# Kernel optimization log

Measured on AMD Instinct MI355X. Metric: run time of the kernel, lower is better.

The kernel has to match this reference:

```python
import jax, jax.numpy as jnp
import numpy as np


def setup_inputs() -> dict:
    key = jax.random.key(0)
    ks = jax.random.split(key, 6)
    b, t, k, h = 2, 2048, 256, 8
    s = 1.0 / np.sqrt(k)
    return {
        "x": jax.random.normal(ks[0], (b, t, k), dtype=jnp.float32),
        "Wq": jax.random.normal(ks[1], (k, k * h), dtype=jnp.float32) * s,
        "Wk": jax.random.normal(ks[2], (k, k * h), dtype=jnp.float32) * s,
        "Wv": jax.random.normal(ks[3], (k, k * h), dtype=jnp.float32) * s,
        "Wu": jax.random.normal(ks[4], (k * h, k), dtype=jnp.float32) * (1.0 / np.sqrt(k * h)),
        "bu": jnp.zeros((k,), dtype=jnp.float32),
    }


def reference(x, Wq, Wk, Wv, Wu, bu):
    b, t, k = x.shape
    h = Wq.shape[1] // k
    scale = k ** (-0.25)
    # projections -> [b, t, h, k] -> [b, h, t, k]
    q = (x @ Wq).reshape(b, t, h, k).transpose(0, 2, 1, 3) * scale
    kk = (x @ Wk).reshape(b, t, h, k).transpose(0, 2, 1, 3) * scale
    v = (x @ Wv).reshape(b, t, h, k).transpose(0, 2, 1, 3)
    dot = jnp.einsum('bhqk,bhsk->bhqs', q, kk)  # [b,h,t,t]
    attn = jax.nn.softmax(dot, axis=-1)
    out = jnp.einsum('bhqs,bhsk->bhqk', attn, v)  # [b,h,t,k]
    out = out.transpose(0, 2, 1, 3).reshape(b, t, h * k)
    return out @ Wu + bu
```

## Files before the change

### kernel.cpp

```cpp
#include <hip/hip_runtime.h>

using bf16x8   = __bf16 __attribute__((ext_vector_type(8)));
using floatx4  = float __attribute__((ext_vector_type(4)));
using floatx16 = float __attribute__((ext_vector_type(16)));

static __device__ __forceinline__ unsigned short f2b(float x) {
  unsigned u = __builtin_bit_cast(unsigned, x);
  u = (u + 0x7fffu + ((u >> 16) & 1u)) >> 16;
  return (unsigned short)u;
}

static __device__ __forceinline__ void gl_lds16(const unsigned short* g, unsigned short* l) {
  __builtin_amdgcn_global_load_lds((const __attribute__((address_space(1))) void*)g,
                                   (__attribute__((address_space(3))) void*)l, 16, 0, 0);
}

__global__ __launch_bounds__(256) void prep_kernel(const float* __restrict__ x,
                                                   const float* __restrict__ Wq,
                                                   const float* __restrict__ Wk,
                                                   const float* __restrict__ Wv,
                                                   const float* __restrict__ Wu,
                                                   unsigned short* __restrict__ xb,
                                                   unsigned short* __restrict__ wqkt,
                                                   unsigned short* __restrict__ wvt,
                                                   unsigned short* __restrict__ wut) {
  int bx = blockIdx.x;
  if (bx < 1024) {
    int i = (bx * 256 + threadIdx.x) * 4;
    float4 v = *(const float4*)(x + i);
    unsigned long long p = (unsigned long long)f2b(v.x) |
                           ((unsigned long long)f2b(v.y) << 16) |
                           ((unsigned long long)f2b(v.z) << 32) |
                           ((unsigned long long)f2b(v.w) << 48);
    *(unsigned long long*)(xb + i) = p;
    return;
  }
  __shared__ unsigned short T[64][65];
  const float* src;
  unsigned short* dst;
  int R, C, tile;
  if (bx < 1152)      { src = Wq; dst = wqkt;          R = 256;  C = 2048; tile = bx - 1024; }
  else if (bx < 1280) { src = Wk; dst = wqkt + 524288; R = 256;  C = 2048; tile = bx - 1152; }
  else if (bx < 1408) { src = Wv; dst = wvt;           R = 256;  C = 2048; tile = bx - 1280; }
  else                { src = Wu; dst = wut;           R = 2048; C = 256;  tile = bx - 1408; }
  int ctiles = C >> 6;
  int cx = tile % ctiles, ry = tile / ctiles;
  int r0 = ry * 64, c0 = cx * 64;
  int t = threadIdx.x;
#pragma unroll
  for (int i = 0; i < 16; ++i) {
    int idx = i * 256 + t;
    int r = idx >> 6, c = idx & 63;
    T[r][c] = f2b(src[(size_t)(r0 + r) * C + c0 + c]);
  }
  __syncthreads();
#pragma unroll
  for (int i = 0; i < 16; ++i) {
    int idx = i * 256 + t;
    int c = idx >> 6, r = idx & 63;
    dst[(size_t)(c0 + c) * R + r0 + r] = T[r][c];
  }
}

__global__ __launch_bounds__(256) void proj_kernel(const unsigned short* __restrict__ A,
                                                   const unsigned short* __restrict__ Bt,
                                                   unsigned short* __restrict__ qkb,
                                                   unsigned short* __restrict__ vtb) {
  __shared__ __align__(16) unsigned short SMEM[128 * 136];
  unsigned short* As = SMEM;
  unsigned short* Bs = SMEM + 4096;
  const int Kt = 256;
  int tid = threadIdx.x, lane = tid & 63, w = tid >> 6;
  int m16 = lane & 15, quad = lane >> 4;
  int wr = w & 1, wc = w >> 1;
  int m0 = blockIdx.y * 128, n0 = blockIdx.x * 128;
  int srow0 = w * 32 + (lane >> 2);
  int schunk = (lane & 3) ^ ((lane >> 2) & 3);
  floatx4 acc[4][4] = {};
  for (int k0 = 0; k0 < Kt; k0 += 32) {
    __syncthreads();
#pragma unroll
    for (int j = 0; j < 2; ++j) {
      int r = srow0 + j * 16;
      gl_lds16(A + (size_t)(m0 + r) * Kt + k0 + schunk * 8, &As[(w * 32 + j * 16) * 32]);
      gl_lds16(Bt + (size_t)(n0 + r) * Kt + k0 + schunk * 8, &Bs[(w * 32 + j * 16) * 32]);
    }
    __syncthreads();
    int sw = (quad ^ (m16 & 3)) * 8;
    bf16x8 af[4], bfr[4];
#pragma unroll
    for (int i = 0; i < 4; ++i) {
      af[i]  = *(const bf16x8*)(&As[(wr * 64 + i * 16 + m16) * 32 + sw]);
      bfr[i] = *(const bf16x8*)(&Bs[(wc * 64 + i * 16 + m16) * 32 + sw]);
    }
#pragma unroll
    for (int i = 0; i < 4; ++i)
#pragma unroll
      for (int jn = 0; jn < 4; ++jn)
        acc[i][jn] = __builtin_amdgcn_mfma_f32_16x16x32_bf16(af[i], bfr[jn], acc[i][jn], 0, 0, 0);
  }
  if (n0 < 4096) {
#pragma unroll
    for (int i = 0; i < 4; ++i)
#pragma unroll
      for (int jn = 0; jn < 4; ++jn)
#pragma unroll
        for (int r = 0; r < 4; ++r) {
          int m = m0 + wr * 64 + i * 16 + quad * 4 + r;
          int n = n0 + wc * 64 + jn * 16 + m16;
          qkb[(size_t)m * 4096 + n] = f2b(acc[i][jn][r]);
        }
  } else {
    __syncthreads();
    unsigned short* Vt = SMEM;
#pragma unroll
    for (int i = 0; i < 4; ++i)
#pragma unroll
      for (int jn = 0; jn < 4; ++jn)
#pragma unroll
        for (int r = 0; r < 4; ++r) {
          int nn = wc * 64 + jn * 16 + m16;
          int mm = wr * 64 + i * 16 + quad * 4 + r;
          Vt[nn * 136 + mm] = f2b(acc[i][jn][r]);
        }
    __syncthreads();
    int bb = m0 >> 11, t0 = m0 & 2047;
#pragma unroll
    for (int i2 = 0; i2 < 8; ++i2) {
      int idx = i2 * 256 + tid;
      int nn = idx >> 4;
      int mc = (idx & 15) * 8;
      uint4 v = *(const uint4*)(&Vt[nn * 136 + mc]);
      *(uint4*)(&vtb[((size_t)(bb * 2048 + n0 - 4096 + nn)) * 2048 + t0 + mc]) = v;
    }
  }
}

__global__ __launch_bounds__(256) void out_kernel(const unsigned short* __restrict__ A,
                                                  const unsigned short* __restrict__ Bt,
                                                  float* __restrict__ Cout,
                                                  const float* __restrict__ bias) {
  __shared__ unsigned short As[64 * 64];
  __shared__ unsigned short Bs[64 * 64];
  const int Kt = 2048;
  int tid = threadIdx.x, lane = tid & 63, w = tid >> 6;
  int m16 = lane & 15, quad = lane >> 4;
  int m0 = blockIdx.y * 64, n0 = blockIdx.x * 64;
  int srow_i = lane >> 3;
  int schunk = (lane & 7) ^ srow_i;
  int rsw = m16 & 7;
  floatx4 acc[4] = {};
  for (int k0 = 0; k0 < Kt; k0 += 64) {
    __syncthreads();
#pragma unroll
    for (int j = 0; j < 2; ++j) {
      int r = w * 16 + j * 8 + srow_i;
      gl_lds16(A + (size_t)(m0 + r) * Kt + k0 + schunk * 8, &As[(w * 16 + j * 8) * 64]);
      gl_lds16(Bt + (size_t)(n0 + r) * Kt + k0 + schunk * 8, &Bs[(w * 16 + j * 8) * 64]);
    }
    __syncthreads();
    bf16x8 af[2];
#pragma unroll
    for (int kk = 0; kk < 2; ++kk)
      af[kk] = *(const bf16x8*)(&As[(w * 16 + m16) * 64 + (((kk * 4 + quad) ^ rsw) * 8)]);
#pragma unroll
    for (int nt = 0; nt < 4; ++nt)
#pragma unroll
      for (int kk = 0; kk < 2; ++kk) {
        bf16x8 bfv = *(const bf16x8*)(&Bs[(nt * 16 + m16) * 64 + (((kk * 4 + quad) ^ rsw) * 8)]);
        acc[nt] = __builtin_amdgcn_mfma_f32_16x16x32_bf16(af[kk], bfv, acc[nt], 0, 0, 0);
      }
  }
#pragma unroll
  for (int nt = 0; nt < 4; ++nt)
#pragma unroll
    for (int r = 0; r < 4; ++r) {
      int m = m0 + w * 16 + quad * 4 + r;
      int n = n0 + nt * 16 + m16;
      Cout[(size_t)m * 256 + n] = acc[nt][r] + bias[n];
    }
}

__global__ __launch_bounds__(512, 2) void attn_kernel(const unsigned short* __restrict__ qk,
                                                      const unsigned short* __restrict__ vt,
                                                      unsigned short* __restrict__ ao) {
  __shared__ __align__(16) unsigned short Ks[2][64 * 256];
  __shared__ __align__(16) unsigned short Vs[2][256 * 64];
  __shared__ __align__(16) unsigned short Pb[4][32 * 72];
  int tid = threadIdx.x, lane = tid & 63, w = tid >> 6;
  int c32 = lane & 31, hi = lane >> 5;
  int qg = w & 3, u = w >> 2;
  int id = blockIdx.x;
  int xcd = id & 7, j = id >> 3;
  int bh = xcd + 8 * (j & 1);
  int q0 = (j >> 1) * 128;
  int b = bh >> 3, h = bh & 7;

  bf16x8 qf[16];
  const unsigned short* qrow =
      qk + (size_t)(b * 2048 + q0 + qg * 32 + c32) * 4096 + h * 256 + hi * 8;
#pragma unroll
  for (int kk = 0; kk < 16; ++kk) qf[kk] = *(const bf16x8*)(qrow + kk * 16);

  bf16x8 onesf;
#pragma unroll
  for (int i = 0; i < 8; ++i) onesf[i] = (__bf16)1.0f;

  floatx16 O[4] = {};
  floatx16 l = {};

  const unsigned short* kbase = qk + (size_t)b * 2048 * 4096 + 2048 + h * 256;
  const unsigned short* vbase = vt + (size_t)bh * 256 * 2048;
  unsigned short* pq = &Pb[qg][0];

  int krow_i = lane >> 5, kpos = lane & 31;
  int vrow_i = lane >> 3, vpos = lane & 7;
  int ksw = c32 & 7;

#pragma unroll
  for (int i = 0; i < 4; ++i) {
    int kr = i * 2 + krow_i;
    gl_lds16(kbase + (size_t)(w * 8 + kr) * 4096 + ((kpos ^ (kr & 7)) * 8),
             &Ks[0][(w * 8 + i * 2) * 256]);
    int vr = i * 8 + vrow_i;
    gl_lds16(vbase + (size_t)(w * 32 + vr) * 2048 + ((vpos ^ vrow_i) * 8),
             &Vs[0][(w * 32 + i * 8) * 64]);
  }

  for (int st = 0; st < 32; ++st) {
    int cur = st & 1;
    __syncthreads();

    floatx16 s = {};
    const unsigned short* krl = &Ks[cur][(u * 32 + c32) * 256];
#pragma unroll
    for (int kk = 0; kk < 16; ++kk) {
      bf16x8 kf = *(const bf16x8*)(krl + (((kk * 2 + hi) ^ ksw) * 8));
      s = __builtin_amdgcn_mfma_f32_32x32x16_bf16(qf[kk], kf, s, 0, 0, 0);
    }
#pragma unroll
    for (int i = 0; i < 16; ++i) {
      float p = __expf(s[i] * 0.0625f);
      int q = (i & 3) + 8 * (i >> 2) + 4 * hi;
      pq[q * 72 + u * 32 + c32] = f2b(p);
    }
    __syncthreads();

    if (st < 31) {
      int s0 = (st + 1) * 64;
      unsigned short* kdst = &Ks[1 - cur][0];
      unsigned short* vdst = &Vs[1 - cur][0];
#pragma unroll
      for (int i = 0; i < 4; ++i) {
        int kr = i * 2 + krow_i;
        gl_lds16(kbase + (size_t)(s0 + w * 8 + kr) * 4096 + ((kpos ^ (kr & 7)) * 8),
                 kdst + (w * 8 + i * 2) * 256);
        int vr = i * 8 + vrow_i;
        gl_lds16(vbase + (size_t)(w * 32 + vr) * 2048 + s0 + ((vpos ^ vrow_i) * 8),
                 vdst + (w * 32 + i * 8) * 64);
      }
    }

    bf16x8 paf[4];
#pragma unroll
    for (int f = 0; f < 4; ++f) paf[f] = *(const bf16x8*)(pq + c32 * 72 + f * 16 + hi * 8);
#pragma unroll
    for (int f = 0; f < 4; ++f)
      l = __builtin_amdgcn_mfma_f32_32x32x16_bf16(paf[f], onesf, l, 0, 0, 0);
#pragma unroll
    for (int dt = 0; dt < 4; ++dt) {
      const unsigned short* vrl = &Vs[cur][(u * 128 + dt * 32 + c32) * 64];
#pragma unroll
      for (int f = 0; f < 4; ++f) {
        bf16x8 vf = *(const bf16x8*)(vrl + (((f * 2 + hi) ^ ksw) * 8));
        O[dt] = __builtin_amdgcn_mfma_f32_32x32x16_bf16(paf[f], vf, O[dt], 0, 0, 0);
      }
    }
  }
  float inv[16];
#pragma unroll
  for (int i = 0; i < 16; ++i) inv[i] = 1.0f / l[i];
#pragma unroll
  for (int dt = 0; dt < 4; ++dt)
#pragma unroll
    for (int i = 0; i < 16; ++i) {
      int q = (i & 3) + 8 * (i >> 2) + 4 * hi;
      ao[(size_t)(b * 2048 + q0 + qg * 32 + q) * 2048 + h * 256 + u * 128 + dt * 32 + c32] =
          f2b(O[dt][i] * inv[i]);
    }
}

extern "C" void kernel_launch(void* const* d_in, const int* in_sizes, int n_in,
                              void* d_out, int out_size, void* d_ws, size_t ws_size,
                              hipStream_t stream) {
  const float* x  = (const float*)d_in[0];
  const float* Wq = (const float*)d_in[1];
  const float* Wk = (const float*)d_in[2];
  const float* Wv = (const float*)d_in[3];
  const float* Wu = (const float*)d_in[4];
  const float* bu = (const float*)d_in[5];

  unsigned short* xb   = (unsigned short*)d_ws;
  unsigned short* wqkt = xb + 1048576;
  unsigned short* wvt  = wqkt + 1048576;
  unsigned short* wut  = wvt + 524288;
  unsigned short* qkb  = wut + 524288;
  unsigned short* vtb  = qkb + 16777216;
  unsigned short* aob  = vtb + 8388608;

  prep_kernel<<<1536, 256, 0, stream>>>(x, Wq, Wk, Wv, Wu, xb, wqkt, wvt, wut);
  proj_kernel<<<dim3(48, 32), 256, 0, stream>>>(xb, wqkt, qkb, vtb);
  attn_kernel<<<256, 512, 0, stream>>>(qkb, vtb, aob);
  out_kernel<<<dim3(4, 64), 256, 0, stream>>>(aob, wut, (float*)d_out, bu);
}
```

Before: 200.9 us.

## Split attention keys across warp pairs and deepen out-GEMM K tile

Measured after the change: 201.3 us. No clear change (+0.2%).

```diff
diff --git a/kernel.cpp b/kernel.cpp
--- a/kernel.cpp
+++ b/kernel.cpp
@@ -140,34 +140,34 @@
                                                   const unsigned short* __restrict__ Bt,
                                                   float* __restrict__ Cout,
                                                   const float* __restrict__ bias) {
-  __shared__ unsigned short As[64 * 64];
-  __shared__ unsigned short Bs[64 * 64];
+  __shared__ unsigned short As[64 * 128];
+  __shared__ unsigned short Bs[64 * 128];
   const int Kt = 2048;
   int tid = threadIdx.x, lane = tid & 63, w = tid >> 6;
   int m16 = lane & 15, quad = lane >> 4;
   int m0 = blockIdx.y * 64, n0 = blockIdx.x * 64;
-  int srow_i = lane >> 3;
-  int schunk = (lane & 7) ^ srow_i;
+  int srow_i = lane >> 4;
+  int spos = lane & 15;
   int rsw = m16 & 7;
   floatx4 acc[4] = {};
-  for (int k0 = 0; k0 < Kt; k0 += 64) {
-    __syncthreads();
-#pragma unroll
-    for (int j = 0; j < 2; ++j) {
-      int r = w * 16 + j * 8 + srow_i;
-      gl_lds16(A + (size_t)(m0 + r) * Kt + k0 + schunk * 8, &As[(w * 16 + j * 8) * 64]);
-      gl_lds16(Bt + (size_t)(n0 + r) * Kt + k0 + schunk * 8, &Bs[(w * 16 + j * 8) * 64]);
-    }
-    __syncthreads();
-    bf16x8 af[2];
-#pragma unroll
-    for (int kk = 0; kk < 2; ++kk)
-      af[kk] = *(const bf16x8*)(&As[(w * 16 + m16) * 64 + (((kk * 4 + quad) ^ rsw) * 8)]);
+  for (int k0 = 0; k0 < Kt; k0 += 128) {
+    __syncthreads();
+#pragma unroll
+    for (int j = 0; j < 4; ++j) {
+      int r = w * 16 + j * 4 + srow_i;
+      gl_lds16(A + (size_t)(m0 + r) * Kt + k0 + ((spos ^ (r & 7)) * 8), &As[(w * 16 + j * 4) * 128]);
+      gl_lds16(Bt + (size_t)(n0 + r) * Kt + k0 + ((spos ^ (r & 7)) * 8), &Bs[(w * 16 + j * 4) * 128]);
+    }
+    __syncthreads();
+    bf16x8 af[4];
+#pragma unroll
+    for (int kk = 0; kk < 4; ++kk)
+      af[kk] = *(const bf16x8*)(&As[(w * 16 + m16) * 128 + (((kk * 4 + quad) ^ rsw) * 8)]);
 #pragma unroll
     for (int nt = 0; nt < 4; ++nt)
 #pragma unroll
-      for (int kk = 0; kk < 2; ++kk) {
-        bf16x8 bfv = *(const bf16x8*)(&Bs[(nt * 16 + m16) * 64 + (((kk * 4 + quad) ^ rsw) * 8)]);
+      for (int kk = 0; kk < 4; ++kk) {
+        bf16x8 bfv = *(const bf16x8*)(&Bs[(nt * 16 + m16) * 128 + (((kk * 4 + quad) ^ rsw) * 8)]);
         acc[nt] = __builtin_amdgcn_mfma_f32_16x16x32_bf16(af[kk], bfv, acc[nt], 0, 0, 0);
       }
   }
@@ -184,12 +184,14 @@
 __global__ __launch_bounds__(512, 2) void attn_kernel(const unsigned short* __restrict__ qk,
                                                       const unsigned short* __restrict__ vt,
                                                       unsigned short* __restrict__ ao) {
-  __shared__ __align__(16) unsigned short Ks[2][64 * 256];
-  __shared__ __align__(16) unsigned short Vs[2][256 * 64];
-  __shared__ __align__(16) unsigned short Pb[4][32 * 72];
+  __shared__ __align__(16) unsigned char SM[150016];
+  unsigned short* KsBuf = (unsigned short*)SM;
+  unsigned short* VsBuf = (unsigned short*)(SM + 65536);
+  float* lsh = (float*)(SM + 149504);
   int tid = threadIdx.x, lane = tid & 63, w = tid >> 6;
   int c32 = lane & 31, hi = lane >> 5;
   int qg = w & 3, u = w >> 2;
+  unsigned short* Pw = (unsigned short*)(SM + 131072) + w * 1152;
   int id = blockIdx.x;
   int xcd = id & 7, j = id >> 3;
   int bh = xcd + 8 * (j & 1);
@@ -202,16 +204,11 @@
 #pragma unroll
   for (int kk = 0; kk < 16; ++kk) qf[kk] = *(const bf16x8*)(qrow + kk * 16);
 
-  bf16x8 onesf;
-#pragma unroll
-  for (int i = 0; i < 8; ++i) onesf[i] = (__bf16)1.0f;
-
-  floatx16 O[4] = {};
-  floatx16 l = {};
+  floatx16 O[8] = {};
+  float lacc = 0.f;
 
   const unsigned short* kbase = qk + (size_t)b * 2048 * 4096 + 2048 + h * 256;
   const unsigned short* vbase = vt + (size_t)bh * 256 * 2048;
-  unsigned short* pq = &Pb[qg][0];
 
   int krow_i = lane >> 5, kpos = lane & 31;
   int vrow_i = lane >> 3, vpos = lane & 7;
@@ -221,73 +218,93 @@
   for (int i = 0; i < 4; ++i) {
     int kr = i * 2 + krow_i;
     gl_lds16(kbase + (size_t)(w * 8 + kr) * 4096 + ((kpos ^ (kr & 7)) * 8),
-             &Ks[0][(w * 8 + i * 2) * 256]);
+             KsBuf + (w * 8 + i * 2) * 256);
     int vr = i * 8 + vrow_i;
     gl_lds16(vbase + (size_t)(w * 32 + vr) * 2048 + ((vpos ^ vrow_i) * 8),
-             &Vs[0][(w * 32 + i * 8) * 64]);
+             VsBuf + (w * 32 + i * 8) * 64);
   }
 
   for (int st = 0; st < 32; ++st) {
     int cur = st & 1;
-    __syncthreads();
-
-    floatx16 s = {};
-    const unsigned short* krl = &Ks[cur][(u * 32 + c32) * 256];
-#pragma unroll
-    for (int kk = 0; kk < 16; ++kk) {
-      bf16x8 kf = *(const bf16x8*)(krl + (((kk * 2 + hi) ^ ksw) * 8));
-      s = __builtin_amdgcn_mfma_f32_32x32x16_bf16(qf[kk], kf, s, 0, 0, 0);
-    }
-#pragma unroll
-    for (int i = 0; i < 16; ++i) {
-      float p = __expf(s[i] * 0.0625f);
-      int q = (i & 3) + 8 * (i >> 2) + 4 * hi;
-      pq[q * 72 + u * 32 + c32] = f2b(p);
-    }
-    __syncthreads();
-
+    unsigned short* Kc = KsBuf + cur * 16384;
+    unsigned short* Vc = VsBuf + cur * 16384;
+    __syncthreads();
     if (st < 31) {
       int s0 = (st + 1) * 64;
-      unsigned short* kdst = &Ks[1 - cur][0];
-      unsigned short* vdst = &Vs[1 - cur][0];
+      unsigned short* kd = KsBuf + (1 - cur) * 16384;
+      unsigned short* vd = VsBuf + (1 - cur) * 16384;
 #pragma unroll
       for (int i = 0; i < 4; ++i) {
         int kr = i * 2 + krow_i;
         gl_lds16(kbase + (size_t)(s0 + w * 8 + kr) * 4096 + ((kpos ^ (kr & 7)) * 8),
-                 kdst + (w * 8 + i * 2) * 256);
+                 kd + (w * 8 + i * 2) * 256);
         int vr = i * 8 + vrow_i;
         gl_lds16(vbase + (size_t)(w * 32 + vr) * 2048 + s0 + ((vpos ^ vrow_i) * 8),
-                 vdst + (w * 32 + i * 8) * 64);
-      }
-    }
-
-    bf16x8 paf[4];
-#pragma unroll
-    for (int f = 0; f < 4; ++f) paf[f] = *(const bf16x8*)(pq + c32 * 72 + f * 16 + hi * 8);
-#pragma unroll
-    for (int f = 0; f < 4; ++f)
-      l = __builtin_amdgcn_mfma_f32_32x32x16_bf16(paf[f], onesf, l, 0, 0, 0);
-#pragma unroll
-    for (int dt = 0; dt < 4; ++dt) {
-      const unsigned short* vrl = &Vs[cur][(u * 128 + dt * 32 + c32) * 64];
-#pragma unroll
-      for (int f = 0; f < 4; ++f) {
-        bf16x8 vf = *(const bf16x8*)(vrl + (((f * 2 + hi) ^ ksw) * 8));
+                 vd + (w * 32 + i * 8) * 64);
+      }
+    }
+
+    floatx16 s = {};
+    const unsigned short* krl = Kc + (u * 32 + c32) * 256;
+#pragma unroll
+    for (int kk = 0; kk < 16; ++kk) {
+      bf16x8 kf = *(const bf16x8*)(krl + (((kk * 2 + hi) ^ ksw) * 8));
+      s = __builtin_amdgcn_mfma_f32_32x32x16_bf16(kf, qf[kk], s, 0, 0, 0);
+    }
+    float lsum = 0.f;
+#pragma unroll
+    for (int i = 0; i < 16; ++i) {
+      float p = __expf(s[i] * 0.0625f);
+      lsum += p;
+      int sl = (i & 3) + 8 * (i >> 2) + 4 * hi;
+      Pw[c32 * 36 + sl] = f2b(p);
+    }
+    lacc += lsum;
+    bf16x8 paf[2];
+#pragma unroll
+    for (int f = 0; f < 2; ++f) paf[f] = *(const bf16x8*)(Pw + c32 * 36 + f * 16 + hi * 8);
+#pragma unroll
+    for (int dt = 0; dt < 8; ++dt) {
+      const unsigned short* vrl = Vc + (dt * 32 + c32) * 64;
+#pragma unroll
+      for (int f = 0; f < 2; ++f) {
+        bf16x8 vf = *(const bf16x8*)(vrl + (((u * 4 + f * 2 + hi) ^ ksw) * 8));
         O[dt] = __builtin_amdgcn_mfma_f32_32x32x16_bf16(paf[f], vf, O[dt], 0, 0, 0);
       }
     }
   }
-  float inv[16];
-#pragma unroll
-  for (int i = 0; i < 16; ++i) inv[i] = 1.0f / l[i];
-#pragma unroll
-  for (int dt = 0; dt < 4; ++dt)
+
+  float lw = lacc + __shfl_xor(lacc, 32);
+  __syncthreads();
+  float* osh = (float*)SM;
+  if (u == 0) {
+    float* od = osh + qg * 8192;
+#pragma unroll
+    for (int dt = 0; dt < 8; ++dt)
+#pragma unroll
+      for (int i = 0; i < 16; ++i) {
+        int q = (i & 3) + 8 * (i >> 2) + 4 * hi;
+        od[q * 256 + dt * 32 + c32] = O[dt][i];
+      }
+    if (hi == 0) lsh[qg * 32 + c32] = lw;
+  }
+  __syncthreads();
+  if (u == 1 && hi == 0) lsh[qg * 32 + c32] += lw;
+  __syncthreads();
+  if (u == 1) {
+    float* od = osh + qg * 8192;
+    unsigned short* aor = ao + (size_t)(b * 2048 + q0 + qg * 32) * 2048 + h * 256;
 #pragma unroll
     for (int i = 0; i < 16; ++i) {
       int q = (i & 3) + 8 * (i >> 2) + 4 * hi;
-      ao[(size_t)(b * 2048 + q0 + qg * 32 + q) * 2048 + h * 256 + u * 128 + dt * 32 + c32] =
-          f2b(O[dt][i] * inv[i]);
-    }
+      float lr = 1.0f / lsh[qg * 32 + q];
+#pragma unroll
+      for (int dt = 0; dt < 8; ++dt) {
+        float v = (O[dt][i] + od[q * 256 + dt * 32 + c32]) * lr;
+        aor[(size_t)q * 2048 + dt * 32 + c32] = f2b(v);
+      }
+    }
+  }
 }
 
 extern "C" void kernel_launch(void* const* d_in, const int* in_sizes, int n_in,
```
